# Kernel optimization log

Hardware: AMD Instinct MI355X
Metric: run time of the kernel (lower is better)

## Reference

```python
import jax, jax.numpy as jnp
import numpy as np
from jax import lax

CONF_THR = 0.1
IOU_THR = 0.45
B, C, IMG = 4, 20, 416.0
SIZES = {"p3": 8112, "p4": 2028, "p5": 507}


def setup_inputs() -> dict:
    key = jax.random.key(0)
    ks = jax.random.split(key, 4 * len(SIZES))
    d = {}
    i = 0
    for name, n in SIZES.items():
        # valid xyxy boxes: random centers in image, widths/heights in [4, 104]
        cxy = jax.random.uniform(ks[i], (B, n, 2), jnp.float32) * IMG
        wh = jax.random.uniform(ks[i + 1], (B, n, 2), jnp.float32) * 100.0 + 4.0
        d[f"{name}_boxes"] = jnp.concatenate([cxy - wh / 2, cxy + wh / 2], axis=-1)
        d[f"{name}_conf"] = jax.random.uniform(ks[i + 2], (B, n, 1), jnp.float32)
        d[f"{name}_cls"] = jax.random.uniform(ks[i + 3], (B, n, C), jnp.float32)
        i += 4
    return d


def _iou_row(b, boxes, area_b, areas):
    # IoU of one box b [4] against all boxes [N,4] (same clamp math as torch _nms)
    xx1 = jnp.maximum(boxes[:, 0], b[0])
    yy1 = jnp.maximum(boxes[:, 1], b[1])
    xx2 = jnp.minimum(boxes[:, 2], b[2])
    yy2 = jnp.minimum(boxes[:, 3], b[3])
    inter = jnp.maximum(xx2 - xx1, 0.0) * jnp.maximum(yy2 - yy1, 0.0)
    return inter / (area_b + areas - inter)


def _nms_keep(boxes, scores, valid):
    # Greedy NMS on one image with padding. Returns (order, keep) so that
    # boxes[order][keep] matches torch's detections[keep-indices] set.
    n = boxes.shape[0]
    order = jnp.argsort(-scores)  # descending, as scores.sort(descending=True)
    sb = boxes[order]
    sv = valid[order]
    areas = (sb[:, 2] - sb[:, 0]) * (sb[:, 3] - sb[:, 1])
    idx = jnp.arange(n)

    def body(i, supp):
        keep_i = jnp.logical_and(sv[i], jnp.logical_not(supp[i]))
        iou = _iou_row(sb[i], sb, areas[i], areas)  # [N]
        return jnp.logical_or(supp, keep_i & (iou > IOU_THR) & (idx > i))

    supp = lax.fori_loop(0, n, body, jnp.zeros(n, bool))
    keep = jnp.logical_and(sv, jnp.logical_not(supp))
    return order, keep


def reference(p3_boxes, p3_conf, p3_cls, p4_boxes, p4_conf, p4_cls,
              p5_boxes, p5_conf, p5_cls):
    boxes = jnp.concatenate([p3_boxes, p4_boxes, p5_boxes], axis=1)   # [B,N,4]
    conf = jnp.concatenate([p3_conf, p4_conf, p5_conf], axis=1)[..., 0]  # [B,N]
    cls = jnp.concatenate([p3_cls, p4_cls, p5_cls], axis=1)           # [B,N,C]

    cls_conf = jnp.max(cls, axis=-1)
    cls_idx = jnp.argmax(cls, axis=-1)
    valid = conf > CONF_THR           # torch drops these; we mask (padded NMS)
    score = jnp.where(valid, conf * cls_conf, 0.0)

    order, keep = jax.vmap(_nms_keep)(boxes, score, valid)  # [B,N] each

    sb = jnp.take_along_axis(boxes, order[..., None], axis=1)
    ss = jnp.take_along_axis(score, order, axis=1)
    sc = jnp.take_along_axis(cls_idx, order, axis=1)
    out_score = jnp.where(keep, ss, 0.0)
    dets = jnp.concatenate(
        [sb, out_score[..., None], sc.astype(jnp.float32)[..., None]], axis=-1
    )  # [B,N,6] = (x1,y1,x2,y2,conf,class), score-sorted; keep marks survivors
    return dets, keep
```

## Files before the change

kernel.cpp:

```cpp
#include <hip/hip_runtime.h>
#include <stdint.h>

#define NB3 8112
#define NB4 2028
#define NB5 507
#define NTOT 10647
#define NBATCH 4
#define NCLS 20
#define NW32 333
#define NW64 167
#define NPAIR 84
#define NTAIL 23
#define LDS_CAP 9984
#define CONF_THR_F 0.1f
#define IOU_THR_F 0.45f
#define IOU_MID ((double)IOU_THR_F + 0x1p-26)

typedef unsigned long long u64;

__global__ void prep_kernel(const float* __restrict__ p3b, const float* __restrict__ p3c, const float* __restrict__ p3k,
                            const float* __restrict__ p4b, const float* __restrict__ p4c, const float* __restrict__ p4k,
                            const float* __restrict__ p5b, const float* __restrict__ p5c, const float* __restrict__ p5k,
                            uint64_t* __restrict__ keys, float4* __restrict__ boxes_cat,
                            float* __restrict__ score, int* __restrict__ clsidx, uint32_t* __restrict__ svout,
                            u64* __restrict__ validbits, int* __restrict__ nvalid)
{
#pragma clang fp contract(off)
    int idx = blockIdx.x * 256 + threadIdx.x;
    if (idx < NBATCH * NW64) validbits[idx] = 0ull;
    if (idx < NBATCH) nvalid[idx] = 0;
    if (idx >= NBATCH * NTOT) return;
    int b = idx / NTOT;
    int i = idx - b * NTOT;

    const float* bx; const float* cf; const float* cl; int n, off;
    if (i < NB3)            { bx = p3b; cf = p3c; cl = p3k; n = NB3; off = i; }
    else if (i < NB3 + NB4) { bx = p4b; cf = p4c; cl = p4k; n = NB4; off = i - NB3; }
    else                    { bx = p5b; cf = p5c; cl = p5k; n = NB5; off = i - NB3 - NB4; }

    size_t e = (size_t)b * n + off;
    float4 box = *(const float4*)(bx + e * 4);
    float conf = cf[e];
    const float* c = cl + e * NCLS;
    float m = c[0]; int mi = 0;
    #pragma unroll
    for (int k = 1; k < NCLS; ++k) { float v = c[k]; if (v > m) { m = v; mi = k; } }

    bool valid = conf > CONF_THR_F;
    float s = valid ? conf * m : 0.0f;
    uint32_t sb = __float_as_uint(s);
    keys[idx]      = ((uint64_t)sb << 32) | (uint32_t)(0xFFFFFFFFu - (uint32_t)i);
    boxes_cat[idx] = box;
    score[idx]     = s;
    clsidx[idx]    = mi;
    svout[idx]     = valid ? 1u : 0u;
}

__global__ void rank_kernel(const uint64_t* __restrict__ keys,
                            const float4* __restrict__ boxes_cat,
                            const float* __restrict__ score,
                            const int* __restrict__ clsidx,
                            const uint32_t* __restrict__ sv,
                            float4* __restrict__ sboxes, float* __restrict__ sscore,
                            int* __restrict__ scls, uint32_t* __restrict__ ssv,
                            u64* __restrict__ validbits, int* __restrict__ nvalid)
{
    int b = blockIdx.y;
    int i = blockIdx.x * 256 + threadIdx.x;
    const uint64_t* kb = keys + (size_t)b * NTOT;
    uint64_t mykey = (i < NTOT) ? kb[i] : 0ull;

    __shared__ uint64_t tile[256];
    int rank = 0;
    for (int t0 = 0; t0 < NTOT; t0 += 256) {
        int j = t0 + threadIdx.x;
        tile[threadIdx.x] = (j < NTOT) ? kb[j] : 0ull;
        __syncthreads();
        #pragma unroll 8
        for (int t = 0; t < 256; ++t) rank += (tile[t] > mykey) ? 1 : 0;
        __syncthreads();
    }

    if (i < NTOT) {
        size_t src = (size_t)b * NTOT + i;
        size_t dst = (size_t)b * NTOT + rank;
        sboxes[dst] = boxes_cat[src];
        sscore[dst] = score[src];
        scls[dst]   = clsidx[src];
        uint32_t v  = sv[src];
        ssv[dst]    = v;
        if (v) {
            atomicOr(&validbits[(size_t)b * NW64 + (rank >> 6)], 1ull << (rank & 63));
            atomicMax(&nvalid[b], rank + 1);
        }
    }
}

__global__ void __launch_bounds__(256) mask_build(const float4* __restrict__ sboxes,
                                                  u64* __restrict__ mask,
                                                  u64* __restrict__ ldiag,
                                                  u64* __restrict__ s1diag,
                                                  u64* __restrict__ s2diag,
                                                  u64* __restrict__ s3diag,
                                                  u64* __restrict__ s4diag,
                                                  u64* __restrict__ s5diag)
{
#pragma clang fp contract(off)
    int c = blockIdx.y;
    if (c < blockIdx.x * 4) return;
    int b = blockIdx.z;
    int sub = threadIdx.x >> 6;
    int lane = threadIdx.x & 63;
    int r = blockIdx.x * 4 + sub;

    __shared__ float4 cb[64];
    __shared__ float  ca[64];
    if (threadIdx.x < 64) {
        int j = c * 64 + threadIdx.x;
        float4 bj = sboxes[(size_t)b * NTOT + (j < NTOT ? j : NTOT - 1)];
        cb[threadIdx.x] = bj;
        ca[threadIdx.x] = (bj.z - bj.x) * (bj.w - bj.y);
    }
    __syncthreads();

    if (r >= NW64 || c < r) return;
    int i = r * 64 + lane;
    float4 bi = sboxes[(size_t)b * NTOT + (i < NTOT ? i : NTOT - 1)];
    float ax1 = bi.x, ay1 = bi.y, ax2 = bi.z, ay2 = bi.w;
    float area_i = (ax2 - ax1) * (ay2 - ay1);

    u64 hh = 0;
    #pragma unroll 8
    for (int k = 0; k < 64; ++k) {
        float4 bj = cb[k];
        float xx1 = fmaxf(bj.x, ax1);
        float yy1 = fmaxf(bj.y, ay1);
        float xx2 = fminf(bj.z, ax2);
        float yy2 = fminf(bj.w, ay2);
        float w = fmaxf(xx2 - xx1, 0.0f);
        float h = fmaxf(yy2 - yy1, 0.0f);
        float inter = w * h;
        float uni = (area_i + ca[k]) - inter;
        bool hit = (double)inter > IOU_MID * (double)uni;
        hh |= (u64)hit << k;
    }

    if (i < NTOT) {
        u64 colmask = (c == NW64 - 1) ? ((1ull << NTAIL) - 1) : ~0ull;
        u64 mw = hh & colmask;
        size_t bl = ((size_t)b * NW64 + r) * 64 + lane;
        if (c == r) {
            u64 gtmask = (lane < 63) ? (~0ull << (lane + 1)) : 0ull;
            mask[((size_t)b * NTOT + i) * NW64 + c] = mw & gtmask;
            ldiag[bl] = hh & ((1ull << lane) - 1);
        } else {
            mask[((size_t)b * NTOT + i) * NW64 + c] = mw;
            if (c == r + 1) s1diag[bl] = mw;
            if (c == r + 2) s2diag[bl] = mw;
            if (c == r + 3) s3diag[bl] = mw;
            if (c == r + 4) s4diag[bl] = mw;
            if (c == r + 5) s5diag[bl] = mw;
        }
    }
}

static __device__ __forceinline__ void bar_sync()
{
    asm volatile("s_waitcnt lgkmcnt(0)" ::: "memory");
    __builtin_amdgcn_s_barrier();
    asm volatile("" ::: "memory");
}

static __device__ __forceinline__ u64 rfl64(u64 x)
{
    uint32_t lo = __builtin_amdgcn_readfirstlane((uint32_t)x);
    uint32_t hi = __builtin_amdgcn_readfirstlane((uint32_t)(x >> 32));
    return ((u64)hi << 32) | (u64)lo;
}

__global__ void __launch_bounds__(1024) resolve_kernel(const u64* __restrict__ mask,
                                                       const u64* __restrict__ ldiag,
                                                       const u64* __restrict__ s1diag,
                                                       const u64* __restrict__ s2diag,
                                                       const u64* __restrict__ s3diag,
                                                       const u64* __restrict__ s4diag,
                                                       const u64* __restrict__ s5diag,
                                                       const u64* __restrict__ validbits,
                                                       const float4* __restrict__ sboxes,
                                                       const float* __restrict__ sscore,
                                                       const int* __restrict__ scls,
                                                       const uint32_t* __restrict__ ssv,
                                                       u64* __restrict__ rem_out,
                                                       float* __restrict__ out)
{
    int b = blockIdx.x;
    int tid = threadIdx.x;
    int lane = tid & 63;
    int wv = tid >> 6;
    const u64* M  = mask   + (size_t)b * NTOT * NW64;
    const u64* LD = ldiag  + (size_t)b * NW64 * 64;
    const u64* S1A = s1diag + (size_t)b * NW64 * 64;
    const u64* S2A = s2diag + (size_t)b * NW64 * 64;
    const u64* S3A = s3diag + (size_t)b * NW64 * 64;
    const u64* S4A = s4diag + (size_t)b * NW64 * 64;
    const u64* S5A = s5diag + (size_t)b * NW64 * 64;
    const u64* V  = validbits + (size_t)b * NW64;

    __shared__ u64 rem_s[NW64 + 1];
    __shared__ u64 v_s[NW64 + 1];
    __shared__ u64 kept_s[2][2];
    __shared__ int klist[2][128];
    __shared__ u64 sc_s;

    for (int t = tid; t < NW64; t += 1024) { rem_s[t] = 0ull; v_s[t] = V[t]; }
    if (tid == 0) {
        rem_s[NW64] = 0ull; v_s[NW64] = 0ull;
        kept_s[0][0] = kept_s[0][1] = kept_s[1][0] = kept_s[1][1] = 0ull;
        klist[0][0] = 0; klist[1][0] = 0; sc_s = 0ull;
    }

    u64 ld0 = 0, s1_0 = 0, s2_0 = 0, s3_0 = 0, s4_0 = 0, s5_0 = 0;
    u64 ld1 = 0, s1_1 = 0, s2_1 = 0, s3_1 = 0, s4_1 = 0;
    if (wv == 0) {
        ld0 = LD[lane];
        s1_0 = S1A[lane]; s2_0 = S2A[lane]; s3_0 = S3A[lane];
        s4_0 = S4A[lane]; s5_0 = S5A[lane];
        ld1 = LD[64 + lane];
        s1_1 = S1A[64 + lane]; s2_1 = S2A[64 + lane];
        s3_1 = S3A[64 + lane]; s4_1 = S4A[64 + lane];
    }

    u64 df[5][3];
    #pragma unroll
    for (int t = 0; t < 5; ++t) {
        #pragma unroll
        for (int c = 0; c < 3; ++c) df[t][c] = 0ull;
    }

    bar_sync();

    for (int p = 0; p < NPAIR; ++p) {
        int par = p & 1;
        int w0 = 2 * p, w1 = 2 * p + 1;

        if (wv == 0) {
            u64 a0pre = rfl64(v_s[w0] & ~rem_s[w0]);
            u64 a1pre = rfl64(v_s[w1] & ~rem_s[w1]);

            u64 U = a0pre, K0 = 0;
            while (U) {
                u64 UK = U | K0;
                bool inU = (U >> lane) & 1;
                u64 nk = __ballot(inU && ((ld0 & UK) == 0ull));
                u64 nr = __ballot(inU && ((ld0 & K0) != 0ull));
                K0 |= nk;
                U &= ~(nk | nr);
            }

            if (lane == 0) sc_s = 0ull;
            if (((K0 >> lane) & 1) && s1_0)
                atomicOr((unsigned long long*)&sc_s, (unsigned long long)s1_0);
            asm volatile("s_waitcnt lgkmcnt(0)" ::: "memory");
            u64 S1 = sc_s;

            u64 U1 = a1pre & ~S1, K1 = 0;
            while (U1) {
                u64 UK = U1 | K1;
                bool inU = (U1 >> lane) & 1;
                u64 nk = __ballot(inU && ((ld1 & UK) == 0ull));
                u64 nr = __ballot(inU && ((ld1 & K1) != 0ull));
                K1 |= nk;
                U1 &= ~(nk | nr);
            }

            if (lane == 0) {
                kept_s[par][0] = K0; kept_s[par][1] = K1;
                u64 sup0 = a0pre & ~K0;
                u64 sup1 = a1pre & ~K1;
                if (sup0) rem_s[w0] |= sup0;
                if (sup1) rem_s[w1] |= sup1;
            }
            int w2 = w0 + 2, w3 = w0 + 3, w4 = w0 + 4, w5 = w0 + 5;
            bool h2 = w2 < NW64, h3 = w3 < NW64, h4 = w4 < NW64, h5 = w5 < NW64;
            if ((K0 >> lane) & 1) {
                if (h2 && s2_0) atomicOr((unsigned long long*)&rem_s[w2], (unsigned long long)s2_0);
                if (h3 && s3_0) atomicOr((unsigned long long*)&rem_s[w3], (unsigned long long)s3_0);
                if (h4 && s4_0) atomicOr((unsigned long long*)&rem_s[w4], (unsigned long long)s4_0);
                if (h5 && s5_0) atomicOr((unsigned long long*)&rem_s[w5], (unsigned long long)s5_0);
            }
            if ((K1 >> lane) & 1) {
                if (h2 && s1_1) atomicOr((unsigned long long*)&rem_s[w2], (unsigned long long)s1_1);
                if (h3 && s2_1) atomicOr((unsigned long long*)&rem_s[w3], (unsigned long long)s2_1);
                if (h4 && s3_1) atomicOr((unsigned long long*)&rem_s[w4], (unsigned long long)s3_1);
                if (h5 && s4_1) atomicOr((unsigned long long*)&rem_s[w5], (unsigned long long)s4_1);
            }
            int pn = (p + 1 < NPAIR) ? p + 1 : p;
            int i0 = 2 * pn;
            int i1 = (2 * pn + 1 < NW64) ? 2 * pn + 1 : NW64 - 1;
            ld0  = LD [(size_t)i0 * 64 + lane];
            s1_0 = S1A[(size_t)i0 * 64 + lane];
            s2_0 = S2A[(size_t)i0 * 64 + lane];
            s3_0 = S3A[(size_t)i0 * 64 + lane];
            s4_0 = S4A[(size_t)i0 * 64 + lane];
            s5_0 = S5A[(size_t)i0 * 64 + lane];
            ld1  = LD [(size_t)i1 * 64 + lane];
            s1_1 = S1A[(size_t)i1 * 64 + lane];
            s2_1 = S2A[(size_t)i1 * 64 + lane];
            s3_1 = S3A[(size_t)i1 * 64 + lane];
            s4_1 = S4A[(size_t)i1 * 64 + lane];
        } else {
            int parw = par ^ 1;
            u64 k0 = kept_s[parw][0], k1 = kept_s[parw][1];
            int n0 = __popcll(k0);
            int nk = n0 + __popcll(k1);
            u64 below = (1ull << lane) - 1;
            if ((k0 >> lane) & 1) klist[parw][__popcll(k0 & below)] = lane;
            if ((k1 >> lane) & 1) klist[parw][n0 + __popcll(k1 & below)] = 64 + lane;

            #pragma unroll
            for (int t = 0; t < 5; ++t) {
                #pragma unroll
                for (int c = 0; c < 3; ++c) {
                    if (df[t][c])
                        atomicOr((unsigned long long*)&rem_s[2 * p + 2 + (c << 6) + lane],
                                 (unsigned long long)df[t][c]);
                }
            }

            int q = (p > 0) ? p - 1 : 0;
            int nkc = (nk < 64) ? nk : 64;
            #pragma unroll
            for (int t = 0; t < 5; ++t) {
                int s = (wv - 1) + t * 15;
                bool has = (p > 0) && (s < nkc);
                int rr = klist[parw][has ? s : 0];
                const u64* R = M + (size_t)(q * 128 + rr) * NW64;
                #pragma unroll
                for (int c = 0; c < 3; ++c) {
                    int w = 2 * q + 6 + (c << 6) + lane;
                    df[t][c] = (has && w < NW64) ? R[w] : 0ull;
                }
            }
            for (int base = 64; base < nk; base += 64) {
                #pragma unroll
                for (int t = 0; t < 5; ++t) {
                    int s = base + (wv - 1) + t * 15;
                    bool has = s < nk;
                    int rr = klist[parw][has ? s : 0];
                    const u64* R = M + (size_t)(q * 128 + rr) * NW64;
                    #pragma unroll
                    for (int c = 0; c < 3; ++c) {
                        int w = 2 * q + 6 + (c << 6) + lane;
                        u64 v2 = (has && w < NW64) ? R[w] : 0ull;
                        if (v2) atomicOr((unsigned long long*)&rem_s[w], (unsigned long long)v2);
                    }
                }
            }
        }

        bar_sync();
    }


    for (int t = tid; t < NW64; t += 1024)
        rem_out[(size_t)b * NW64 + t] = rem_s[t];

    for (int t = tid; t < NTOT; t += 1024) {
        size_t idx = (size_t)b * NTOT + t;
        float4 box = sboxes[idx];
        u64 rw = rem_s[t >> 6];
        bool keep = (ssv[idx] != 0u) && !((rw >> (t & 63)) & 1ull);
        float sc = keep ? sscore[idx] : 0.0f;
        float* d = out + idx * 6;
        d[0] = box.x; d[1] = box.y; d[2] = box.z; d[3] = box.w;
        d[4] = sc;    d[5] = (float)scls[idx];
        out[(size_t)NBATCH * NTOT * 6 + idx] = keep ? 1.0f : 0.0f;
    }
}

extern __shared__ unsigned char nms_smem[];

__global__ void __launch_bounds__(1024) nms_kernel(const float4* __restrict__ sboxes,
                                                   const uint32_t* __restrict__ ssv,
                                                   const int* __restrict__ nvalid_arr,
                                                   uint32_t* __restrict__ supp_out)
{
#pragma clang fp contract(off)
    int b = blockIdx.x;
    float4*   lbox = (float4*)nms_smem;
    uint32_t* supp = (uint32_t*)(nms_smem + (size_t)LDS_CAP * 16);
    uint32_t* svb  = supp + NW32;

    int nv = nvalid_arr[b];
    const float4* gb = sboxes + (size_t)b * NTOT;
    const uint32_t* gv = ssv + (size_t)b * NTOT;

    for (int t = threadIdx.x; t < NW32; t += 1024) { supp[t] = 0u; svb[t] = 0u; }
    __syncthreads();
    for (int t = threadIdx.x; t < nv; t += 1024) {
        if (t < LDS_CAP) lbox[t] = gb[t];
        if (gv[t]) atomicOr(&svb[t >> 5], 1u << (t & 31));
    }
    __syncthreads();

    for (int i = 0; i < nv; ++i) {
        uint32_t sw = supp[i >> 5];
        if ((sw >> (i & 31)) & 1u) continue;
        uint32_t vw = svb[i >> 5];
        if (!((vw >> (i & 31)) & 1u)) continue;

        float4 bi = (i < LDS_CAP) ? lbox[i] : gb[i];
        float ax1 = bi.x, ay1 = bi.y, ax2 = bi.z, ay2 = bi.w;
        float area_i = (ax2 - ax1) * (ay2 - ay1);

        for (int j = i + 1 + (int)threadIdx.x; j < nv; j += 1024) {
            float4 bj = (j < LDS_CAP) ? lbox[j] : gb[j];
            float xx1 = fmaxf(bj.x, ax1);
            float yy1 = fmaxf(bj.y, ay1);
            float xx2 = fminf(bj.z, ax2);
            float yy2 = fminf(bj.w, ay2);
            float w = fmaxf(xx2 - xx1, 0.0f);
            float h = fmaxf(yy2 - yy1, 0.0f);
            float inter  = w * h;
            float area_j = (bj.z - bj.x) * (bj.w - bj.y);
            float iou = inter / ((area_i + area_j) - inter);
            if (iou > IOU_THR_F) atomicOr(&supp[j >> 5], 1u << (j & 31));
        }
        __syncthreads();
    }

    __syncthreads();
    for (int t = threadIdx.x; t < NW32; t += 1024)
        supp_out[(size_t)b * (2 * NW64) + t] = supp[t];
}

__global__ void out_kernel(const float4* __restrict__ sboxes, const float* __restrict__ sscore,
                           const int* __restrict__ scls, const uint32_t* __restrict__ ssv,
                           const u64* __restrict__ rem, float* __restrict__ out)
{
    int idx = blockIdx.x * 256 + threadIdx.x;
    if (idx >= NBATCH * NTOT) return;
    int b = idx / NTOT;
    int p = idx - b * NTOT;

    float4 box = sboxes[idx];
    u64 rw = rem[(size_t)b * NW64 + (p >> 6)];
    bool keep = (ssv[idx] != 0u) && !((rw >> (p & 63)) & 1ull);
    float sc = keep ? sscore[idx] : 0.0f;

    float* d = out + (size_t)idx * 6;
    d[0] = box.x; d[1] = box.y; d[2] = box.z; d[3] = box.w;
    d[4] = sc;    d[5] = (float)scls[idx];
    out[(size_t)NBATCH * NTOT * 6 + idx] = keep ? 1.0f : 0.0f;
}

extern "C" void kernel_launch(void* const* d_in, const int* in_sizes, int n_in,
                              void* d_out, int out_size, void* d_ws, size_t ws_size,
                              hipStream_t stream)
{
    const float* p3b = (const float*)d_in[0];
    const float* p3c = (const float*)d_in[1];
    const float* p3k = (const float*)d_in[2];
    const float* p4b = (const float*)d_in[3];
    const float* p4c = (const float*)d_in[4];
    const float* p4k = (const float*)d_in[5];
    const float* p5b = (const float*)d_in[6];
    const float* p5c = (const float*)d_in[7];
    const float* p5k = (const float*)d_in[8];
    float* out = (float*)d_out;

    char* ws = (char*)d_ws;
    size_t off = 0;
    auto alloc = [&](size_t bytes) { size_t o = off; off += (bytes + 255) & ~(size_t)255; return o; };
    const size_t BN = (size_t)NBATCH * NTOT;
    uint64_t* keys      = (uint64_t*)(ws + alloc(BN * 8));
    float4*   boxes_cat = (float4*)  (ws + alloc(BN * 16));
    float*    score     = (float*)   (ws + alloc(BN * 4));
    int*      clsidx    = (int*)     (ws + alloc(BN * 4));
    uint32_t* sv        = (uint32_t*)(ws + alloc(BN * 4));
    float4*   sboxes    = (float4*)  (ws + alloc(BN * 16));
    float*    sscore    = (float*)   (ws + alloc(BN * 4));
    int*      scls      = (int*)     (ws + alloc(BN * 4));
    uint32_t* ssv       = (uint32_t*)(ws + alloc(BN * 4));
    u64*      rem64     = (u64*)     (ws + alloc((size_t)NBATCH * NW64 * 8));
    u64*      validbits = (u64*)     (ws + alloc((size_t)NBATCH * NW64 * 8));
    int*      nvalid    = (int*)     (ws + alloc(NBATCH * 4));
    u64*      ldiag     = (u64*)     (ws + alloc((size_t)NBATCH * NW64 * 64 * 8));
    u64*      s1diag    = (u64*)     (ws + alloc((size_t)NBATCH * NW64 * 64 * 8));
    u64*      s2diag    = (u64*)     (ws + alloc((size_t)NBATCH * NW64 * 64 * 8));
    u64*      s3diag    = (u64*)     (ws + alloc((size_t)NBATCH * NW64 * 64 * 8));
    u64*      s4diag    = (u64*)     (ws + alloc((size_t)NBATCH * NW64 * 64 * 8));
    u64*      s5diag    = (u64*)     (ws + alloc((size_t)NBATCH * NW64 * 64 * 8));
    u64*      mask      = (u64*)     (ws + alloc((size_t)NBATCH * NTOT * NW64 * 8));
    bool fast = (off <= ws_size);

    int nblk = (int)((BN + 255) / 256);
    prep_kernel<<<nblk, 256, 0, stream>>>(p3b, p3c, p3k, p4b, p4c, p4k, p5b, p5c, p5k,
                                          keys, boxes_cat, score, clsidx, sv,
                                          validbits, nvalid);

    dim3 rgrid((NTOT + 255) / 256, NBATCH);
    rank_kernel<<<rgrid, 256, 0, stream>>>(keys, boxes_cat, score, clsidx, sv,
                                           sboxes, sscore, scls, ssv, validbits, nvalid);

    if (fast) {
        dim3 mgrid((NW64 + 3) / 4, NW64, NBATCH);
        mask_build<<<mgrid, 256, 0, stream>>>(sboxes, mask, ldiag, s1diag, s2diag,
                                              s3diag, s4diag, s5diag);
        resolve_kernel<<<NBATCH, 1024, 0, stream>>>(mask, ldiag, s1diag, s2diag, s3diag,
                                                    s4diag, s5diag, validbits,
                                                    sboxes, sscore, scls, ssv,
                                                    rem64, out);
    } else {
        hipMemsetAsync(rem64, 0, (size_t)NBATCH * NW64 * 8, stream);
        size_t smem = (size_t)LDS_CAP * 16 + (size_t)NW32 * 4 * 2;
        smem = (smem + 15) & ~(size_t)15;
        hipFuncSetAttribute((const void*)nms_kernel, hipFuncAttributeMaxDynamicSharedMemorySize, (int)smem);
        nms_kernel<<<NBATCH, 1024, smem, stream>>>(sboxes, ssv, nvalid, (uint32_t*)rem64);
        out_kernel<<<nblk, 256, 0, stream>>>(sboxes, sscore, scls, ssv, rem64, out);
    }
}
```

Baseline: 522.6 us.

## Split rank counting across key slices with atomic accumulation, separate scatter

The O(N^2) rank computation is split across key slices (RSL=6 slices of 7 tiles each), and each thread now ranks 4 keys so every loaded LDS tile entry is reused four times. Partial counts are accumulated with atomicAdd into a rank array zeroed in prep, and a separate scatter kernel permutes the data. This adds parallelism and register-level reuse in the comparison loop. The cost is one extra kernel launch, global atomics and an extra rank array round-trip.

```diff
diff --git a/kernel.cpp b/kernel.cpp
--- a/kernel.cpp
+++ b/kernel.cpp
@@ -11,6 +11,9 @@
 #define NW64 167
 #define NPAIR 84
 #define NTAIL 23
+#define RCH 11
+#define RSL 6
+#define RTP 7
 #define LDS_CAP 9984
 #define CONF_THR_F 0.1f
 #define IOU_THR_F 0.45f
@@ -23,13 +26,14 @@
                             const float* __restrict__ p5b, const float* __restrict__ p5c, const float* __restrict__ p5k,
                             uint64_t* __restrict__ keys, float4* __restrict__ boxes_cat,
                             float* __restrict__ score, int* __restrict__ clsidx, uint32_t* __restrict__ svout,
-                            u64* __restrict__ validbits, int* __restrict__ nvalid)
+                            u64* __restrict__ validbits, int* __restrict__ nvalid, int* __restrict__ rank)
 {
 #pragma clang fp contract(off)
     int idx = blockIdx.x * 256 + threadIdx.x;
     if (idx < NBATCH * NW64) validbits[idx] = 0ull;
     if (idx < NBATCH) nvalid[idx] = 0;
     if (idx >= NBATCH * NTOT) return;
+    rank[idx] = 0;
     int b = idx / NTOT;
     int i = idx - b * NTOT;
 
@@ -56,43 +60,63 @@
     svout[idx]     = valid ? 1u : 0u;
 }
 
-__global__ void rank_kernel(const uint64_t* __restrict__ keys,
-                            const float4* __restrict__ boxes_cat,
-                            const float* __restrict__ score,
-                            const int* __restrict__ clsidx,
-                            const uint32_t* __restrict__ sv,
-                            float4* __restrict__ sboxes, float* __restrict__ sscore,
-                            int* __restrict__ scls, uint32_t* __restrict__ ssv,
-                            u64* __restrict__ validbits, int* __restrict__ nvalid)
-{
-    int b = blockIdx.y;
-    int i = blockIdx.x * 256 + threadIdx.x;
+__global__ void __launch_bounds__(256) rank_partial(const uint64_t* __restrict__ keys,
+                                                    int* __restrict__ rank)
+{
+    int b = blockIdx.z;
     const uint64_t* kb = keys + (size_t)b * NTOT;
-    uint64_t mykey = (i < NTOT) ? kb[i] : 0ull;
+    int i0 = blockIdx.x * 1024 + threadIdx.x;
+    uint64_t k0 = (i0       < NTOT) ? kb[i0]       : 0ull;
+    uint64_t k1 = (i0 + 256 < NTOT) ? kb[i0 + 256] : 0ull;
+    uint64_t k2 = (i0 + 512 < NTOT) ? kb[i0 + 512] : 0ull;
+    uint64_t k3 = (i0 + 768 < NTOT) ? kb[i0 + 768] : 0ull;
+    int r0 = 0, r1 = 0, r2 = 0, r3 = 0;
 
     __shared__ uint64_t tile[256];
-    int rank = 0;
-    for (int t0 = 0; t0 < NTOT; t0 += 256) {
-        int j = t0 + threadIdx.x;
+    for (int tt = 0; tt < RTP; ++tt) {
+        int j = (blockIdx.y * RTP + tt) * 256 + threadIdx.x;
         tile[threadIdx.x] = (j < NTOT) ? kb[j] : 0ull;
         __syncthreads();
         #pragma unroll 8
-        for (int t = 0; t < 256; ++t) rank += (tile[t] > mykey) ? 1 : 0;
+        for (int t = 0; t < 256; ++t) {
+            uint64_t kt = tile[t];
+            r0 += (kt > k0) ? 1 : 0;
+            r1 += (kt > k1) ? 1 : 0;
+            r2 += (kt > k2) ? 1 : 0;
+            r3 += (kt > k3) ? 1 : 0;
+        }
         __syncthreads();
     }
 
-    if (i < NTOT) {
-        size_t src = (size_t)b * NTOT + i;
-        size_t dst = (size_t)b * NTOT + rank;
-        sboxes[dst] = boxes_cat[src];
-        sscore[dst] = score[src];
-        scls[dst]   = clsidx[src];
-        uint32_t v  = sv[src];
-        ssv[dst]    = v;
-        if (v) {
-            atomicOr(&validbits[(size_t)b * NW64 + (rank >> 6)], 1ull << (rank & 63));
-            atomicMax(&nvalid[b], rank + 1);
-        }
+    int* rb = rank + (size_t)b * NTOT;
+    if (i0       < NTOT) atomicAdd(&rb[i0],       r0);
+    if (i0 + 256 < NTOT) atomicAdd(&rb[i0 + 256], r1);
+    if (i0 + 512 < NTOT) atomicAdd(&rb[i0 + 512], r2);
+    if (i0 + 768 < NTOT) atomicAdd(&rb[i0 + 768], r3);
+}
+
+__global__ void scatter_kernel(const int* __restrict__ rank,
+                               const float4* __restrict__ boxes_cat,
+                               const float* __restrict__ score,
+                               const int* __restrict__ clsidx,
+                               const uint32_t* __restrict__ sv,
+                               float4* __restrict__ sboxes, float* __restrict__ sscore,
+                               int* __restrict__ scls, uint32_t* __restrict__ ssv,
+                               u64* __restrict__ validbits, int* __restrict__ nvalid)
+{
+    int idx = blockIdx.x * 256 + threadIdx.x;
+    if (idx >= NBATCH * NTOT) return;
+    int b = idx / NTOT;
+    int rk = rank[idx];
+    size_t dst = (size_t)b * NTOT + rk;
+    sboxes[dst] = boxes_cat[idx];
+    sscore[dst] = score[idx];
+    scls[dst]   = clsidx[idx];
+    uint32_t v  = sv[idx];
+    ssv[dst]    = v;
+    if (v) {
+        atomicOr(&validbits[(size_t)b * NW64 + (rk >> 6)], 1ull << (rk & 63));
+        atomicMax(&nvalid[b], rk + 1);
     }
 }
 
@@ -478,6 +502,7 @@
     float*    score     = (float*)   (ws + alloc(BN * 4));
     int*      clsidx    = (int*)     (ws + alloc(BN * 4));
     uint32_t* sv        = (uint32_t*)(ws + alloc(BN * 4));
+    int*      rank_arr  = (int*)     (ws + alloc(BN * 4));
     float4*   sboxes    = (float4*)  (ws + alloc(BN * 16));
     float*    sscore    = (float*)   (ws + alloc(BN * 4));
     int*      scls      = (int*)     (ws + alloc(BN * 4));
@@ -497,11 +522,13 @@
     int nblk = (int)((BN + 255) / 256);
     prep_kernel<<<nblk, 256, 0, stream>>>(p3b, p3c, p3k, p4b, p4c, p4k, p5b, p5c, p5k,
                                           keys, boxes_cat, score, clsidx, sv,
-                                          validbits, nvalid);
-
-    dim3 rgrid((NTOT + 255) / 256, NBATCH);
-    rank_kernel<<<rgrid, 256, 0, stream>>>(keys, boxes_cat, score, clsidx, sv,
-                                           sboxes, sscore, scls, ssv, validbits, nvalid);
+                                          validbits, nvalid, rank_arr);
+
+    dim3 rpgrid(RCH, RSL, NBATCH);
+    rank_partial<<<rpgrid, 256, 0, stream>>>(keys, rank_arr);
+
+    scatter_kernel<<<nblk, 256, 0, stream>>>(rank_arr, boxes_cat, score, clsidx, sv,
+                                             sboxes, sscore, scls, ssv, validbits, nvalid);
 
     if (fast) {
         dim3 mgrid((NW64 + 3) / 4, NW64, NBATCH);
```

Result: slower. 863.1 us (+65.1%).
